# Kernel tuning notes

Measured on AMD Instinct MI355X. Metric: run time of the kernel, lower is better.

Reference implementation:

```python
import jax, jax.numpy as jnp
import numpy as np

FG_IOU = 0.7
BG_IOU = 0.3
IMG_H = 640.0
IMG_W = 640.0


def setup_inputs() -> dict:
    key = jax.random.key(0)
    k1, k2, k3, k4 = jax.random.split(key, 4)
    B, A, G = 8, 184320, 64
    # anchors in cxcywh (as the torch module assumes before box_convert)
    cxcy = jax.random.uniform(k1, (B, A, 2), dtype=jnp.float32) * 640.0
    wh = 16.0 + jax.random.uniform(k2, (B, A, 2), dtype=jnp.float32) * 240.0
    anchors = jnp.concatenate([cxcy, wh], axis=-1)
    # gt boxes in xyxy, inside the 640x640 image
    xy1 = jax.random.uniform(k3, (B, G, 2), dtype=jnp.float32) * 560.0
    wh_g = 24.0 + jax.random.uniform(k4, (B, G, 2), dtype=jnp.float32) * 180.0
    gt_boxes = jnp.concatenate([xy1, jnp.minimum(xy1 + wh_g, 640.0)], axis=-1)
    return {"anchors": anchors, "gt_boxes": gt_boxes}


def cxcywh_to_xyxy(b):
    cx, cy, w, h = b[..., 0], b[..., 1], b[..., 2], b[..., 3]
    return jnp.stack([cx - 0.5 * w, cy - 0.5 * h, cx + 0.5 * w, cy + 0.5 * h], axis=-1)


def box_iou(a, g):
    # a: [A,4] xyxy, g: [G,4] xyxy -> [A,G]
    area_a = (a[:, 2] - a[:, 0]) * (a[:, 3] - a[:, 1])
    area_g = (g[:, 2] - g[:, 0]) * (g[:, 3] - g[:, 1])
    lt = jnp.maximum(a[:, None, :2], g[None, :, :2])   # [A,G,2]
    rb = jnp.minimum(a[:, None, 2:], g[None, :, 2:])
    wh = jnp.clip(rb - lt, 0.0)
    inter = wh[..., 0] * wh[..., 1]
    return inter / (area_a[:, None] + area_g[None, :] - inter)


def _assign_one(anchors_cxcywh, gt):
    # anchors_cxcywh: [A,4], gt: [G,4] xyxy
    A = anchors_cxcywh.shape[0]
    a = cxcywh_to_xyxy(anchors_cxcywh)                 # [A,4]
    iou = box_iou(a, gt)                               # [A,G]

    labels = jnp.full((A,), -1, dtype=jnp.int32)
    matched = jnp.zeros((A, 4), dtype=anchors_cxcywh.dtype)

    # rule 1: for each gt, the anchor attaining its max IoU is positive
    best_anchor = jnp.argmax(iou, axis=0)              # [G]
    labels = labels.at[best_anchor].set(1)
    matched = matched.at[best_anchor].set(gt)

    # rule 2: anchors with max IoU over gts > fg threshold are positive
    max_gt = jnp.argmax(iou, axis=1)                   # [A]
    max_val = jnp.max(iou, axis=1)                     # [A]
    fg = max_val > FG_IOU
    labels = jnp.where(fg, 1, labels)
    matched = jnp.where(fg[:, None], gt[max_gt], matched)

    # rule 3: remaining anchors with max IoU < bg threshold are negative
    bg = (max_val < BG_IOU) & (labels < 0)
    labels = jnp.where(bg, 0, labels)

    # filter cross-boundary anchors -> ignore label
    cross = (a[:, 0] < 0) | (a[:, 1] < 0) | (a[:, 2] > IMG_W) | (a[:, 3] > IMG_H)
    labels = jnp.where(cross, -1, labels)
    return labels, matched, max_val


def reference(anchors, gt_boxes):
    # anchors: [B,A,4] cxcywh, gt_boxes: [B,G,4] xyxy
    labels, matched_bboxes, max_iou = jax.vmap(_assign_one)(anchors, gt_boxes)
    return labels, matched_bboxes, max_iou
```

## Files before the change

### kernel.cpp

```cpp
#include <hip/hip_runtime.h>


constexpr int B = 8;
constexpr int G = 64;
constexpr int BLOCK = 256;
constexpr int APT = 2;
constexpr int ABLK = BLOCK * APT;
constexpr float IMG = 640.0f;
constexpr float FG_IOU = 0.7f;
constexpr float BG_IOU = 0.3f;
constexpr float SLACK = 1.0f;
constexpr unsigned long long KEY_INIT = 0xFFFFFFFFull;


__global__ __launch_bounds__(256) void build_tables(
    const float4* __restrict__ gt, unsigned long long* __restrict__ tabs) {
    __shared__ float4 sgt[G];
    const int b = blockIdx.x;
    const int t = threadIdx.x;
    if (t < G) sgt[t] = gt[b * G + t];
    __syncthreads();
    const int tabIdx = t >> 6;
    const int strip = t & 63;
    const int comp = (tabIdx == 0) ? 0 : (tabIdx == 1) ? 2 : (tabIdx == 2) ? 1 : 3;
    const bool hi = (tabIdx & 1) != 0;
    const float thr = hi ? (strip * 10.0f - SLACK)
                         : ((strip + 1) * 10.0f + SLACK);
    unsigned long long m = 0ull;
    for (int g = 0; g < G; ++g) {
        float c = ((const float*)&sgt[g])[comp];
        bool in = hi ? (c > thr) : (c < thr);
        if (in) m |= (1ull << g);
    }
    tabs[(b * 4 + tabIdx) * G + strip] = m;
}

__global__ __launch_bounds__(BLOCK) void assign_main(
    const float4* __restrict__ anchors,
    const float4* __restrict__ gt,
    float* __restrict__ L,
    float4* __restrict__ M,
    float* __restrict__ V,
    long long* __restrict__ gkeys,
    const unsigned long long* __restrict__ tabs,
    int A, int bpb) {
#pragma clang fp contract(off)
    __shared__ float4 sgt[G];
    __shared__ float sarea[G];
    __shared__ unsigned long long tab[4][G];
    __shared__ unsigned long long skey[G];

    const int b = blockIdx.x / bpb;
    const int t = threadIdx.x;
    const int base = (blockIdx.x % bpb) * ABLK;

    if (t < G) {
        float4 gb = gt[b * G + t];
        sgt[t] = gb;
        sarea[t] = (gb.z - gb.x) * (gb.w - gb.y);
        skey[t] = KEY_INIT;
    }
    tab[t >> 6][t & 63] = tabs[b * 256 + t];
    __syncthreads();

#pragma unroll
    for (int j = 0; j < APT; ++j) {
        const int a = base + j * BLOCK + t;
        const size_t idx = (size_t)b * A + a;
        float4 an = anchors[idx];
        float ax0 = an.x - 0.5f * an.z;
        float ay0 = an.y - 0.5f * an.w;
        float ax1 = an.x + 0.5f * an.z;
        float ay1 = an.y + 0.5f * an.w;
        float area_a = (ax1 - ax0) * (ay1 - ay0);

        int sx0 = (int)(ax0 * 0.1f); sx0 = sx0 < 0 ? 0 : (sx0 > 63 ? 63 : sx0);
        int sx1 = (int)(ax1 * 0.1f); sx1 = sx1 < 0 ? 0 : (sx1 > 63 ? 63 : sx1);
        int sy0 = (int)(ay0 * 0.1f); sy0 = sy0 < 0 ? 0 : (sy0 > 63 ? 63 : sy0);
        int sy1 = (int)(ay1 * 0.1f); sy1 = sy1 < 0 ? 0 : (sy1 > 63 ? 63 : sy1);

        unsigned long long mask =
            tab[0][sx1] & tab[1][sx0] & tab[2][sy1] & tab[3][sy0];

        float maxv = 0.0f;
        int maxg = 0;
        const unsigned long long inv_p =
            (unsigned long long)(0xFFFFFFFFu - (unsigned)a);

        while (mask) {
            const int g = __ffsll(mask) - 1;
            mask &= mask - 1;
            float4 gb = sgt[g];
            float sa = sarea[g];
            float lx = fmaxf(ax0, gb.x);
            float ly = fmaxf(ay0, gb.y);
            float rx = fminf(ax1, gb.z);
            float ry = fminf(ay1, gb.w);
            float w = fmaxf(rx - lx, 0.0f);
            float h = fmaxf(ry - ly, 0.0f);
            float inter = w * h;
            float uni = area_a + sa - inter;
            float iou = inter / uni;

            bool better = iou > maxv;
            maxv = better ? iou : maxv;
            maxg = better ? g : maxg;

            if (iou > 0.0f) {
                unsigned long long key =
                    ((unsigned long long)__float_as_uint(iou) << 32) | inv_p;
                atomicMax(&skey[g], key);
            }
        }

        bool fg = maxv > FG_IOU;
        bool bg = maxv < BG_IOU;
        bool cross = (ax0 < 0.0f) || (ay0 < 0.0f) || (ax1 > IMG) || (ay1 > IMG);

        L[idx] = cross ? -1.0f : (fg ? 1.0f : (bg ? 0.0f : -1.0f));
        M[idx] = fg ? sgt[maxg] : make_float4(0.0f, 0.0f, 0.0f, 0.0f);
        V[idx] = maxv;
    }

    __syncthreads();
    if (t < G) {
        atomicMax(&gkeys[b * G + t], (long long)skey[t]);
    }
}

__global__ void fixup(
    const float4* __restrict__ anchors,
    const float4* __restrict__ gt,
    const long long* __restrict__ gkeys,
    float* __restrict__ L,
    float4* __restrict__ M,
    const float* __restrict__ V,
    int A) {
#pragma clang fp contract(off)
    const int b = blockIdx.x;
    const int g = threadIdx.x;
    __shared__ int tgt[G];

    unsigned long long key = (unsigned long long)gkeys[b * G + g];
    unsigned int a = 0xFFFFFFFFu - (unsigned int)(key & 0xFFFFFFFFull);
    tgt[g] = (int)a;
    __syncthreads();

    bool write = true;
    for (int g2 = g + 1; g2 < G; ++g2)
        if (tgt[g2] == (int)a) { write = false; break; }
    if (!write) return;

    const size_t idx = (size_t)b * A + a;
    float4 an = anchors[idx];
    float ax0 = an.x - 0.5f * an.z;
    float ay0 = an.y - 0.5f * an.w;
    float ax1 = an.x + 0.5f * an.z;
    float ay1 = an.y + 0.5f * an.w;
    bool cross = (ax0 < 0.0f) || (ay0 < 0.0f) || (ax1 > IMG) || (ay1 > IMG);
    L[idx] = cross ? -1.0f : 1.0f;
    if (!(V[idx] > FG_IOU)) M[idx] = gt[b * G + g];
}

extern "C" void kernel_launch(void* const* d_in, const int* in_sizes, int n_in,
                              void* d_out, int out_size, void* d_ws, size_t ws_size,
                              hipStream_t stream) {
    const float4* anchors = (const float4*)d_in[0];
    const float4* gt      = (const float4*)d_in[1];
    const int A = in_sizes[0] / (B * 4);

    float* out = (float*)d_out;
    float*  L = out;
    float4* M = (float4*)(out + (size_t)B * A);
    float*  V = out + (size_t)B * A * 5;

    char* ws = (char*)d_ws;
    long long* gkeys = (long long*)(ws + 256);
    unsigned long long* tabs = (unsigned long long*)(ws + 8192);

    const int bpb = A / ABLK;
    build_tables<<<B, 256, 0, stream>>>(gt, tabs);
    assign_main<<<B * bpb, BLOCK, 0, stream>>>(anchors, gt, L, M, V, gkeys,
                                               tabs, A, bpb);
    fixup<<<B, G, 0, stream>>>(anchors, gt, gkeys, L, M, V, A);
}
```

Measured before the change: 124.6 us.

## Refine spatial strip tables to 5px and split GT candidate loop into 32-bit halves

Doubles the number of spatial strips in the per-batch GT bitmask tables, from 64 strips of 10px to 128 strips of 5px. Finer strips should produce tighter candidate masks, so fewer anchor–GT IoUs are evaluated. The candidate loop now walks two 32-bit halves with ctz instead of a 64-bit ffsll. GT coordinates move to structure-of-arrays shared memory, and the atomicMax is made unconditional with a zero key, replacing the branch. The cost is twice the table loading per block plus an atomic issued for every candidate, including ones with zero IoU.

```diff
diff --git a/kernel.cpp b/kernel.cpp
--- a/kernel.cpp
+++ b/kernel.cpp
@@ -6,6 +6,9 @@
 constexpr int BLOCK = 256;
 constexpr int APT = 2;
 constexpr int ABLK = BLOCK * APT;
+constexpr int NSTRIP = 128;
+constexpr float STRIP_SCALE = 0.2f;
+constexpr float STRIP_W = 5.0f;
 constexpr float IMG = 640.0f;
 constexpr float FG_IOU = 0.7f;
 constexpr float BG_IOU = 0.3f;
@@ -13,26 +16,26 @@
 constexpr unsigned long long KEY_INIT = 0xFFFFFFFFull;
 
 
-__global__ __launch_bounds__(256) void build_tables(
+__global__ __launch_bounds__(512) void build_tables(
     const float4* __restrict__ gt, unsigned long long* __restrict__ tabs) {
     __shared__ float4 sgt[G];
     const int b = blockIdx.x;
     const int t = threadIdx.x;
     if (t < G) sgt[t] = gt[b * G + t];
     __syncthreads();
-    const int tabIdx = t >> 6;
-    const int strip = t & 63;
+    const int tabIdx = t >> 7;
+    const int strip = t & 127;
     const int comp = (tabIdx == 0) ? 0 : (tabIdx == 1) ? 2 : (tabIdx == 2) ? 1 : 3;
     const bool hi = (tabIdx & 1) != 0;
-    const float thr = hi ? (strip * 10.0f - SLACK)
-                         : ((strip + 1) * 10.0f + SLACK);
+    const float thr = hi ? (strip * STRIP_W - SLACK)
+                         : ((strip + 1) * STRIP_W + SLACK);
     unsigned long long m = 0ull;
     for (int g = 0; g < G; ++g) {
         float c = ((const float*)&sgt[g])[comp];
         bool in = hi ? (c > thr) : (c < thr);
         if (in) m |= (1ull << g);
     }
-    tabs[(b * 4 + tabIdx) * G + strip] = m;
+    tabs[(size_t)b * 512 + t] = m;
 }
 
 __global__ __launch_bounds__(BLOCK) void assign_main(
@@ -46,8 +49,8 @@
     int A, int bpb) {
 #pragma clang fp contract(off)
     __shared__ float4 sgt[G];
-    __shared__ float sarea[G];
-    __shared__ unsigned long long tab[4][G];
+    __shared__ float sgx0[G], sgy0[G], sgx1[G], sgy1[G], sga[G];
+    __shared__ unsigned long long tab[4][NSTRIP];
     __shared__ unsigned long long skey[G];
 
     const int b = blockIdx.x / bpb;
@@ -57,10 +60,15 @@
     if (t < G) {
         float4 gb = gt[b * G + t];
         sgt[t] = gb;
-        sarea[t] = (gb.z - gb.x) * (gb.w - gb.y);
+        sgx0[t] = gb.x; sgy0[t] = gb.y; sgx1[t] = gb.z; sgy1[t] = gb.w;
+        sga[t] = (gb.z - gb.x) * (gb.w - gb.y);
         skey[t] = KEY_INIT;
     }
-    tab[t >> 6][t & 63] = tabs[b * 256 + t];
+    {
+        unsigned long long* tflat = &tab[0][0];
+        tflat[t]       = tabs[(size_t)b * 512 + t];
+        tflat[t + 256] = tabs[(size_t)b * 512 + 256 + t];
+    }
     __syncthreads();
 
 #pragma unroll
@@ -74,10 +82,10 @@
         float ay1 = an.y + 0.5f * an.w;
         float area_a = (ax1 - ax0) * (ay1 - ay0);
 
-        int sx0 = (int)(ax0 * 0.1f); sx0 = sx0 < 0 ? 0 : (sx0 > 63 ? 63 : sx0);
-        int sx1 = (int)(ax1 * 0.1f); sx1 = sx1 < 0 ? 0 : (sx1 > 63 ? 63 : sx1);
-        int sy0 = (int)(ay0 * 0.1f); sy0 = sy0 < 0 ? 0 : (sy0 > 63 ? 63 : sy0);
-        int sy1 = (int)(ay1 * 0.1f); sy1 = sy1 < 0 ? 0 : (sy1 > 63 ? 63 : sy1);
+        int sx0 = (int)(ax0 * STRIP_SCALE); sx0 = sx0 < 0 ? 0 : (sx0 > 127 ? 127 : sx0);
+        int sx1 = (int)(ax1 * STRIP_SCALE); sx1 = sx1 < 0 ? 0 : (sx1 > 127 ? 127 : sx1);
+        int sy0 = (int)(ay0 * STRIP_SCALE); sy0 = sy0 < 0 ? 0 : (sy0 > 127 ? 127 : sy0);
+        int sy1 = (int)(ay1 * STRIP_SCALE); sy1 = sy1 < 0 ? 0 : (sy1 > 127 ? 127 : sy1);
 
         unsigned long long mask =
             tab[0][sx1] & tab[1][sx0] & tab[2][sy1] & tab[3][sy0];
@@ -87,38 +95,46 @@
         const unsigned long long inv_p =
             (unsigned long long)(0xFFFFFFFFu - (unsigned)a);
 
-        while (mask) {
-            const int g = __ffsll(mask) - 1;
-            mask &= mask - 1;
-            float4 gb = sgt[g];
-            float sa = sarea[g];
-            float lx = fmaxf(ax0, gb.x);
-            float ly = fmaxf(ay0, gb.y);
-            float rx = fminf(ax1, gb.z);
-            float ry = fminf(ay1, gb.w);
-            float w = fmaxf(rx - lx, 0.0f);
-            float h = fmaxf(ry - ly, 0.0f);
-            float inter = w * h;
-            float uni = area_a + sa - inter;
-            float iou = inter / uni;
-
-            bool better = iou > maxv;
-            maxv = better ? iou : maxv;
-            maxg = better ? g : maxg;
-
-            if (iou > 0.0f) {
+        unsigned mlo = (unsigned)mask;
+        unsigned mhi = (unsigned)(mask >> 32);
+        auto half = [&](unsigned m, int gbase) {
+            while (m) {
+                const int g = gbase + __builtin_ctz(m);
+                m &= m - 1;
+                float gx0 = sgx0[g], gy0 = sgy0[g];
+                float gx1 = sgx1[g], gy1 = sgy1[g];
+                float sa = sga[g];
+                float lx = fmaxf(ax0, gx0);
+                float ly = fmaxf(ay0, gy0);
+                float rx = fminf(ax1, gx1);
+                float ry = fminf(ay1, gy1);
+                float w = fmaxf(rx - lx, 0.0f);
+                float h = fmaxf(ry - ly, 0.0f);
+                float inter = w * h;
+                float uni = area_a + sa - inter;
+                float iou = inter / uni;
+
+                bool better = iou > maxv;
+                maxv = better ? iou : maxv;
+                maxg = better ? g : maxg;
+
                 unsigned long long key =
                     ((unsigned long long)__float_as_uint(iou) << 32) | inv_p;
+                key = (iou > 0.0f) ? key : 0ull;
                 atomicMax(&skey[g], key);
             }
-        }
+        };
+        half(mlo, 0);
+        half(mhi, 32);
 
         bool fg = maxv > FG_IOU;
         bool bg = maxv < BG_IOU;
         bool cross = (ax0 < 0.0f) || (ay0 < 0.0f) || (ax1 > IMG) || (ay1 > IMG);
 
         L[idx] = cross ? -1.0f : (fg ? 1.0f : (bg ? 0.0f : -1.0f));
-        M[idx] = fg ? sgt[maxg] : make_float4(0.0f, 0.0f, 0.0f, 0.0f);
+        float4 m = make_float4(0.0f, 0.0f, 0.0f, 0.0f);
+        if (fg) m = sgt[maxg];
+        M[idx] = m;
         V[idx] = maxv;
     }
 
@@ -179,7 +195,7 @@
     unsigned long long* tabs = (unsigned long long*)(ws + 8192);
 
     const int bpb = A / ABLK;
-    build_tables<<<B, 256, 0, stream>>>(gt, tabs);
+    build_tables<<<B, 512, 0, stream>>>(gt, tabs);
     assign_main<<<B * bpb, BLOCK, 0, stream>>>(anchors, gt, L, M, V, gkeys,
                                                tabs, A, bpb);
     fixup<<<B, G, 0, stream>>>(anchors, gt, gkeys, L, M, V, A);
```

Result: no change. 122.2 us (-2.0%).
